# Kernel optimization log

Measured on AMD Instinct MI355X. Metric: run time of the kernel, lower is better.

## Reference

```python
import jax, jax.numpy as jnp
import numpy as np

EMBED_DIM = 1024


def setup_inputs() -> dict:
    key = jax.random.key(0)
    ks = jax.random.split(key, 8)
    B, S, D = 4, 2048, EMBED_DIM
    scale = 1.0 / np.sqrt(D)
    x = jax.random.normal(ks[0], (B, S, D), dtype=jnp.float32)
    mask = jnp.zeros((S, S), dtype=jnp.float32)
    # nn.Linear default init ~ U(-1/sqrt(fan_in), 1/sqrt(fan_in)); exact dist irrelevant for correctness
    w_q = jax.random.uniform(ks[1], (D, D), jnp.float32, -scale, scale)
    b_q = jax.random.uniform(ks[2], (D,), jnp.float32, -scale, scale)
    w_k = jax.random.uniform(ks[3], (D, D), jnp.float32, -scale, scale)
    b_k = jax.random.uniform(ks[4], (D,), jnp.float32, -scale, scale)
    w_v = jax.random.uniform(ks[5], (D, D), jnp.float32, -scale, scale)
    b_v = jax.random.uniform(ks[6], (D,), jnp.float32, -scale, scale)
    return {"x": x, "mask": mask, "w_q": w_q, "b_q": b_q,
            "w_k": w_k, "b_k": b_k, "w_v": w_v, "b_v": b_v}


def reference(x, mask, w_q, b_q, w_k, b_k, w_v, b_v):
    D = x.shape[-1]
    # nn.Linear computes x @ W^T + b
    Q = jnp.einsum('bsd,ed->bse', x, w_q) + b_q
    K = jnp.einsum('bsd,ed->bse', x, w_k) + b_k
    V = jnp.einsum('bsd,ed->bse', x, w_v) + b_v
    scores = jnp.einsum('bqd,bkd->bqk', Q, K) / jnp.sqrt(jnp.asarray(D, x.dtype))
    scores = scores + mask  # additive mask, broadcast over batch
    attn = jax.nn.softmax(scores, axis=-1)
    return jnp.einsum('bqk,bkd->bqd', attn, V)
```

## Files before the change

### kernel.cpp

```cpp
#include <hip/hip_runtime.h>


typedef __attribute__((ext_vector_type(8))) short short8;
typedef __attribute__((ext_vector_type(4))) short short4v;
typedef __attribute__((ext_vector_type(4))) float float4v;
typedef __attribute__((ext_vector_type(16))) float float16v;

__device__ __forceinline__ short f2bf(float f) {
  unsigned u = __builtin_bit_cast(unsigned, f);
  u += 0x7fffu + ((u >> 16) & 1u);
  return (short)(u >> 16);
}
__device__ __forceinline__ float bf2f(short s) {
  unsigned u = ((unsigned)(unsigned short)s) << 16;
  return __builtin_bit_cast(float, u);
}

__device__ __forceinline__ void gl2lds16(const void* g, void* l) {
  __builtin_amdgcn_global_load_lds((const __attribute__((address_space(1))) void*)g,
                                   (__attribute__((address_space(3))) void*)l, 16, 0, 0);
}

__global__ __launch_bounds__(256) void cvt_kernel(const float* __restrict__ in,
                                                  short* __restrict__ out, int n4) {
  int i = blockIdx.x * 256 + threadIdx.x;
  if (i < n4) {
    float4v v = ((const float4v*)in)[i];
    short4v o;
    o.x = f2bf(v.x); o.y = f2bf(v.y); o.z = f2bf(v.z); o.w = f2bf(v.w);
    ((short4v*)out)[i] = o;
  }
}

__global__ __launch_bounds__(256) void prep_kernel(const float* __restrict__ wq,
                                                   const float* __restrict__ wk,
                                                   const float* __restrict__ wv,
                                                   const float* __restrict__ bq,
                                                   const float* __restrict__ bk,
                                                   short* __restrict__ w_bf,
                                                   float* __restrict__ bcat) {
  int b = blockIdx.x;
  if (b < 3072) {
    int seg = b >> 10;
    const float* w = seg == 0 ? wq : (seg == 1 ? wk : wv);
    int i = (b - (seg << 10)) * 256 + threadIdx.x;
    float4v v = ((const float4v*)w)[i];
    short4v o;
    o.x = f2bf(v.x); o.y = f2bf(v.y); o.z = f2bf(v.z); o.w = f2bf(v.w);
    ((short4v*)(w_bf + (long)seg * 1048576))[i] = o;
  } else {
    int i = (b - 3072) * 256 + threadIdx.x;
    if (i < 2048) bcat[i] = i < 1024 ? bq[i] : bk[i - 1024];
  }
}

template <int EPI>
__global__ __launch_bounds__(256) void gemm_bt(const short* __restrict__ Aall,
                                               const short* __restrict__ Ball,
                                               void* __restrict__ Call,
                                               const float* __restrict__ aux, float scale,
                                               int M, int N, int Kd, int Bld,
                                               long ab, long bb, long cb, long auxb) {
  const int bz = blockIdx.z;
  const short* A = Aall + (long)bz * ab;
  const short* Bm = Ball + (long)bz * bb;
  const float* auxp = aux + (long)bz * auxb;

  const int m0 = blockIdx.x * 128;
  const int n0 = blockIdx.y * 128;

  __shared__ alignas(16) short As[128][64];
  __shared__ alignas(16) short Bs[128][64];

  const int t = threadIdx.x;
  const int lane = t & 63, wave = t >> 6;
  const int wm = (wave & 1) * 64, wn = (wave >> 1) * 64;
  const int col32 = lane & 31, half = lane >> 5;

  const int r_loc = lane >> 3;
  const int slot = lane & 7;
  const int cch = slot ^ r_loc;
  const int sw = col32 & 7;

  float16v acc[2][2] = {};

  for (int kt = 0; kt < Kd; kt += 64) {
#pragma unroll
    for (int u = 0; u < 4; ++u) {
      const int rowbase = wave * 32 + u * 8;
      const int r = rowbase + r_loc;
      gl2lds16(&A[(long)(m0 + r) * Kd + kt + cch * 8], &As[rowbase][0] + lane * 8);
      gl2lds16(&Bm[(long)(n0 + r) * Bld + kt + cch * 8], &Bs[rowbase][0] + lane * 8);
    }
    __syncthreads();

#pragma unroll
    for (int s = 0; s < 4; ++s) {
      const int c = s * 2 + half;
      short8 af[2], bfr[2];
#pragma unroll
      for (int i = 0; i < 2; ++i)
        af[i] = *(const short8*)&As[wm + i * 32 + col32][(c ^ sw) * 8];
#pragma unroll
      for (int j = 0; j < 2; ++j)
        bfr[j] = *(const short8*)&Bs[wn + j * 32 + col32][(c ^ sw) * 8];
#pragma unroll
      for (int i = 0; i < 2; ++i)
#pragma unroll
        for (int j = 0; j < 2; ++j)
          acc[i][j] = __builtin_amdgcn_mfma_f32_32x32x16_bf16(af[i], bfr[j], acc[i][j], 0, 0, 0);
    }
    __syncthreads();
  }

  const float LOG2E = 1.44269504f;
  const float c1 = scale * LOG2E;
#pragma unroll
  for (int i = 0; i < 2; ++i) {
    float invv[16], addm[16];
    if (EPI == 2) {
#pragma unroll
      for (int r = 0; r < 16; ++r) {
        const int m = m0 + wm + i * 32 + (r & 3) + 8 * (r >> 2) + 4 * half;
        invv[r] = __builtin_amdgcn_rcpf(auxp[m]);
      }
    }
    if (EPI == 3) {
#pragma unroll
      for (int r = 0; r < 16; ++r) {
        const int m = m0 + wm + i * 32 + (r & 3) + 8 * (r >> 2) + 4 * half;
        addm[r] = auxp[m];
      }
    }
#pragma unroll
    for (int j = 0; j < 2; ++j) {
      const int n = n0 + wn + j * 32 + col32;
      float addn = 0.f;
      if (EPI == 0) addn = auxp[n];
#pragma unroll
      for (int r = 0; r < 16; ++r) {
        const int m = m0 + wm + i * 32 + (r & 3) + 8 * (r >> 2) + 4 * half;
        float v = acc[i][j][r];
        if (EPI == 0) {
          ((short*)Call)[(long)bz * cb + (long)m * N + n] = f2bf(v + addn);
        } else if (EPI == 1) {
          float mv = auxp[(long)m * N + n];
          float e = exp2f(fmaf(v, c1, mv * LOG2E));
          ((short*)Call)[(long)bz * cb + (long)m * N + n] = f2bf(e);
        } else if (EPI == 2) {
          ((float*)Call)[(long)bz * cb + (long)m * N + n] = v * invv[r];
        } else {
          ((short*)Call)[(long)bz * cb + (long)m * N + n] = f2bf(v + addm[r]);
        }
      }
    }
  }
}

__global__ __launch_bounds__(256) void rowsum_kernel(const short* __restrict__ P,
                                                     float* __restrict__ rs) {
  const long row = blockIdx.x;
  const int t = threadIdx.x;
  short8 raw = *(const short8*)(P + row * 2048 + t * 8);
  float s = 0.f;
#pragma unroll
  for (int e = 0; e < 8; ++e) s += bf2f(raw[e]);
#pragma unroll
  for (int off = 32; off > 0; off >>= 1) s += __shfl_xor(s, off);
  __shared__ float red[4];
  if ((t & 63) == 0) red[t >> 6] = s;
  __syncthreads();
  if (t == 0) rs[row] = red[0] + red[1] + red[2] + red[3];
}

extern "C" void kernel_launch(void* const* d_in, const int* in_sizes, int n_in,
                              void* d_out, int out_size, void* d_ws, size_t ws_size,
                              hipStream_t stream) {
  const float* x    = (const float*)d_in[0];
  const float* mask = (const float*)d_in[1];
  const float* wq   = (const float*)d_in[2];
  const float* bq   = (const float*)d_in[3];
  const float* wk   = (const float*)d_in[4];
  const float* bk   = (const float*)d_in[5];
  const float* wv   = (const float*)d_in[6];
  const float* bv   = (const float*)d_in[7];
  float* out = (float*)d_out;

  char* ws = (char*)d_ws;
  const size_t MB = 1024 * 1024;
  short* x_bf = (short*)(ws);
  short* w_bf = (short*)(ws + 16 * MB);
  float* rs   = (float*)(ws + 16 * MB);
  short* QK   = (short*)(ws + 22 * MB);
  short* Vt   = (short*)(ws + 54 * MB);
  short* P    = (short*)(ws + 70 * MB);
  float* bcat = (float*)(ws + 70 * MB);

  prep_kernel<<<3080, 256, 0, stream>>>(wq, wk, wv, bq, bk, w_bf, bcat);
  cvt_kernel<<<8192, 256, 0, stream>>>(x, x_bf, 2097152);

  gemm_bt<0><<<dim3(64, 8, 2), 256, 0, stream>>>(x_bf, w_bf, QK, bcat, 1.f,
                                                 8192, 1024, 1024, 1024,
                                                 0, 1048576, 8388608, 1024);

  gemm_bt<3><<<dim3(8, 64, 1), 256, 0, stream>>>(w_bf + 2097152, x_bf, Vt, bv, 1.f,
                                                 1024, 8192, 1024, 1024,
                                                 0, 0, 0, 0);

  short* Q  = QK;
  short* Kb = QK + 8388608;

  gemm_bt<1><<<dim3(16, 16, 4), 256, 0, stream>>>(Q, Kb, P, mask, 0.03125f,
                                                  2048, 2048, 1024, 1024,
                                                  2097152, 2097152, 4194304, 0);

  rowsum_kernel<<<8192, 256, 0, stream>>>(P, rs);

  gemm_bt<2><<<dim3(16, 8, 4), 256, 0, stream>>>(P, Vt, out, rs, 1.f,
                                                 2048, 1024, 2048, 8192,
                                                 4194304, 2048, 2097152, 2048);
}
```

Before: 277.9 us.

## Use 16x16 MFMA tiles, fuse rowsum into score GEMM, merge prep kernels

Switches the GEMM inner loop from 32x32x16 to 16x16x32 bf16 MFMA with a 4x4 accumulator grid per wave. Folds the row-sum of exp scores into the score GEMM epilogue through shuffle reductions and atomicAdd, which removes the separate rowsum pass over P. Also merges the x conversion into the weight prep kernel and adds a small kernel to zero the row sums. Atomics make the summation order nondeterministic, and the new epilogue stores are narrower and more numerous.

```diff
diff --git a/kernel.cpp b/kernel.cpp
--- a/kernel.cpp
+++ b/kernel.cpp
@@ -4,7 +4,6 @@
 typedef __attribute__((ext_vector_type(8))) short short8;
 typedef __attribute__((ext_vector_type(4))) short short4v;
 typedef __attribute__((ext_vector_type(4))) float float4v;
-typedef __attribute__((ext_vector_type(16))) float float16v;
 
 __device__ __forceinline__ short f2bf(float f) {
   unsigned u = __builtin_bit_cast(unsigned, f);
@@ -21,22 +20,13 @@
                                    (__attribute__((address_space(3))) void*)l, 16, 0, 0);
 }
 
-__global__ __launch_bounds__(256) void cvt_kernel(const float* __restrict__ in,
-                                                  short* __restrict__ out, int n4) {
-  int i = blockIdx.x * 256 + threadIdx.x;
-  if (i < n4) {
-    float4v v = ((const float4v*)in)[i];
-    short4v o;
-    o.x = f2bf(v.x); o.y = f2bf(v.y); o.z = f2bf(v.z); o.w = f2bf(v.w);
-    ((short4v*)out)[i] = o;
-  }
-}
-
-__global__ __launch_bounds__(256) void prep_kernel(const float* __restrict__ wq,
+__global__ __launch_bounds__(256) void prep_kernel(const float* __restrict__ x,
+                                                   const float* __restrict__ wq,
                                                    const float* __restrict__ wk,
                                                    const float* __restrict__ wv,
                                                    const float* __restrict__ bq,
                                                    const float* __restrict__ bk,
+                                                   short* __restrict__ x_bf,
                                                    short* __restrict__ w_bf,
                                                    float* __restrict__ bcat) {
   int b = blockIdx.x;
@@ -48,17 +38,28 @@
     short4v o;
     o.x = f2bf(v.x); o.y = f2bf(v.y); o.z = f2bf(v.z); o.w = f2bf(v.w);
     ((short4v*)(w_bf + (long)seg * 1048576))[i] = o;
+  } else if (b < 11264) {
+    int i = (b - 3072) * 256 + threadIdx.x;
+    float4v v = ((const float4v*)x)[i];
+    short4v o;
+    o.x = f2bf(v.x); o.y = f2bf(v.y); o.z = f2bf(v.z); o.w = f2bf(v.w);
+    ((short4v*)x_bf)[i] = o;
   } else {
-    int i = (b - 3072) * 256 + threadIdx.x;
+    int i = (b - 11264) * 256 + threadIdx.x;
     if (i < 2048) bcat[i] = i < 1024 ? bq[i] : bk[i - 1024];
   }
+}
+
+__global__ __launch_bounds__(256) void zero_rs(float* __restrict__ rs) {
+  rs[blockIdx.x * 256 + threadIdx.x] = 0.f;
 }
 
 template <int EPI>
 __global__ __launch_bounds__(256) void gemm_bt(const short* __restrict__ Aall,
                                                const short* __restrict__ Ball,
                                                void* __restrict__ Call,
-                                               const float* __restrict__ aux, float scale,
+                                               const float* __restrict__ aux,
+                                               float* __restrict__ rsum, float scale,
                                                int M, int N, int Kd, int Bld,
                                                long ab, long bb, long cb, long auxb) {
   const int bz = blockIdx.z;
@@ -75,14 +76,14 @@
   const int t = threadIdx.x;
   const int lane = t & 63, wave = t >> 6;
   const int wm = (wave & 1) * 64, wn = (wave >> 1) * 64;
-  const int col32 = lane & 31, half = lane >> 5;
+  const int col = lane & 15, quad = lane >> 4;
 
   const int r_loc = lane >> 3;
   const int slot = lane & 7;
   const int cch = slot ^ r_loc;
-  const int sw = col32 & 7;
-
-  float16v acc[2][2] = {};
+  const int sw = col & 7;
+
+  float4v acc[4][4] = {};
 
   for (int kt = 0; kt < Kd; kt += 64) {
 #pragma unroll
@@ -95,20 +96,19 @@
     __syncthreads();
 
 #pragma unroll
-    for (int s = 0; s < 4; ++s) {
-      const int c = s * 2 + half;
-      short8 af[2], bfr[2];
-#pragma unroll
-      for (int i = 0; i < 2; ++i)
-        af[i] = *(const short8*)&As[wm + i * 32 + col32][(c ^ sw) * 8];
-#pragma unroll
-      for (int j = 0; j < 2; ++j)
-        bfr[j] = *(const short8*)&Bs[wn + j * 32 + col32][(c ^ sw) * 8];
-#pragma unroll
-      for (int i = 0; i < 2; ++i)
-#pragma unroll
-        for (int j = 0; j < 2; ++j)
-          acc[i][j] = __builtin_amdgcn_mfma_f32_32x32x16_bf16(af[i], bfr[j], acc[i][j], 0, 0, 0);
+    for (int s = 0; s < 2; ++s) {
+      short8 af[4], bfr[4];
+#pragma unroll
+      for (int i = 0; i < 4; ++i)
+        af[i] = *(const short8*)&As[wm + i * 16 + col][((s * 4 + quad) ^ sw) * 8];
+#pragma unroll
+      for (int j = 0; j < 4; ++j)
+        bfr[j] = *(const short8*)&Bs[wn + j * 16 + col][((s * 4 + quad) ^ sw) * 8];
+#pragma unroll
+      for (int i = 0; i < 4; ++i)
+#pragma unroll
+        for (int j = 0; j < 4; ++j)
+          acc[i][j] = __builtin_amdgcn_mfma_f32_16x16x32_bf16(af[i], bfr[j], acc[i][j], 0, 0, 0);
     }
     __syncthreads();
   }
@@ -116,37 +116,34 @@
   const float LOG2E = 1.44269504f;
   const float c1 = scale * LOG2E;
 #pragma unroll
-  for (int i = 0; i < 2; ++i) {
-    float invv[16], addm[16];
+  for (int i = 0; i < 4; ++i) {
+    float invv[4], addm[4], rsum4[4] = {0.f, 0.f, 0.f, 0.f};
     if (EPI == 2) {
 #pragma unroll
-      for (int r = 0; r < 16; ++r) {
-        const int m = m0 + wm + i * 32 + (r & 3) + 8 * (r >> 2) + 4 * half;
-        invv[r] = __builtin_amdgcn_rcpf(auxp[m]);
-      }
+      for (int r = 0; r < 4; ++r)
+        invv[r] = __builtin_amdgcn_rcpf(auxp[m0 + wm + i * 16 + quad * 4 + r]);
     }
     if (EPI == 3) {
 #pragma unroll
-      for (int r = 0; r < 16; ++r) {
-        const int m = m0 + wm + i * 32 + (r & 3) + 8 * (r >> 2) + 4 * half;
-        addm[r] = auxp[m];
-      }
-    }
-#pragma unroll
-    for (int j = 0; j < 2; ++j) {
-      const int n = n0 + wn + j * 32 + col32;
+      for (int r = 0; r < 4; ++r) addm[r] = auxp[m0 + wm + i * 16 + quad * 4 + r];
+    }
+#pragma unroll
+    for (int j = 0; j < 4; ++j) {
+      const int n = n0 + wn + j * 16 + col;
       float addn = 0.f;
       if (EPI == 0) addn = auxp[n];
 #pragma unroll
-      for (int r = 0; r < 16; ++r) {
-        const int m = m0 + wm + i * 32 + (r & 3) + 8 * (r >> 2) + 4 * half;
+      for (int r = 0; r < 4; ++r) {
+        const int m = m0 + wm + i * 16 + quad * 4 + r;
         float v = acc[i][j][r];
         if (EPI == 0) {
           ((short*)Call)[(long)bz * cb + (long)m * N + n] = f2bf(v + addn);
         } else if (EPI == 1) {
           float mv = auxp[(long)m * N + n];
           float e = exp2f(fmaf(v, c1, mv * LOG2E));
-          ((short*)Call)[(long)bz * cb + (long)m * N + n] = f2bf(e);
+          short q = f2bf(e);
+          ((short*)Call)[(long)bz * cb + (long)m * N + n] = q;
+          rsum4[r] += bf2f(q);
         } else if (EPI == 2) {
           ((float*)Call)[(long)bz * cb + (long)m * N + n] = v * invv[r];
         } else {
@@ -154,23 +151,21 @@
         }
       }
     }
+    if (EPI == 1) {
+#pragma unroll
+      for (int r = 0; r < 4; ++r) {
+        float s = rsum4[r];
+        s += __shfl_xor(s, 1);
+        s += __shfl_xor(s, 2);
+        s += __shfl_xor(s, 4);
+        s += __shfl_xor(s, 8);
+        if (col == 0) {
+          const int m = m0 + wm + i * 16 + quad * 4 + r;
+          atomicAdd(&rsum[(long)bz * M + m], s);
+        }
+      }
+    }
   }
-}
-
-__global__ __launch_bounds__(256) void rowsum_kernel(const short* __restrict__ P,
-                                                     float* __restrict__ rs) {
-  const long row = blockIdx.x;
-  const int t = threadIdx.x;
-  short8 raw = *(const short8*)(P + row * 2048 + t * 8);
-  float s = 0.f;
-#pragma unroll
-  for (int e = 0; e < 8; ++e) s += bf2f(raw[e]);
-#pragma unroll
-  for (int off = 32; off > 0; off >>= 1) s += __shfl_xor(s, off);
-  __shared__ float red[4];
-  if ((t & 63) == 0) red[t >> 6] = s;
-  __syncthreads();
-  if (t == 0) rs[row] = red[0] + red[1] + red[2] + red[3];
 }
 
 extern "C" void kernel_launch(void* const* d_in, const int* in_sizes, int n_in,
@@ -196,27 +191,26 @@
   short* P    = (short*)(ws + 70 * MB);
   float* bcat = (float*)(ws + 70 * MB);
 
-  prep_kernel<<<3080, 256, 0, stream>>>(wq, wk, wv, bq, bk, w_bf, bcat);
-  cvt_kernel<<<8192, 256, 0, stream>>>(x, x_bf, 2097152);
-
-  gemm_bt<0><<<dim3(64, 8, 2), 256, 0, stream>>>(x_bf, w_bf, QK, bcat, 1.f,
+  prep_kernel<<<11272, 256, 0, stream>>>(x, wq, wk, wv, bq, bk, x_bf, w_bf, bcat);
+
+  gemm_bt<0><<<dim3(64, 8, 2), 256, 0, stream>>>(x_bf, w_bf, QK, bcat, nullptr, 1.f,
                                                  8192, 1024, 1024, 1024,
                                                  0, 1048576, 8388608, 1024);
 
-  gemm_bt<3><<<dim3(8, 64, 1), 256, 0, stream>>>(w_bf + 2097152, x_bf, Vt, bv, 1.f,
+  gemm_bt<3><<<dim3(8, 64, 1), 256, 0, stream>>>(w_bf + 2097152, x_bf, Vt, bv, nullptr, 1.f,
                                                  1024, 8192, 1024, 1024,
                                                  0, 0, 0, 0);
 
+  zero_rs<<<32, 256, 0, stream>>>(rs);
+
   short* Q  = QK;
   short* Kb = QK + 8388608;
 
-  gemm_bt<1><<<dim3(16, 16, 4), 256, 0, stream>>>(Q, Kb, P, mask, 0.03125f,
+  gemm_bt<1><<<dim3(16, 16, 4), 256, 0, stream>>>(Q, Kb, P, mask, rs, 0.03125f,
                                                   2048, 2048, 1024, 1024,
                                                   2097152, 2097152, 4194304, 0);
 
-  rowsum_kernel<<<8192, 256, 0, stream>>>(P, rs);
-
-  gemm_bt<2><<<dim3(16, 8, 4), 256, 0, stream>>>(P, Vt, out, rs, 1.f,
+  gemm_bt<2><<<dim3(16, 8, 4), 256, 0, stream>>>(P, Vt, out, rs, nullptr, 1.f,
                                                  2048, 1024, 2048, 8192,
                                                  4194304, 2048, 2097152, 2048);
 }
```

New measurement: 278.8 us. No clear change (+0.3%).
